# Optimization experiments

Hardware: AMD Instinct MI355X
Metric: run time of the kernel (lower is better)

Reference implementation:

```python
import jax, jax.numpy as jnp
import numpy as np

MASK_VALUE = -1000000.0  # matches torch source's value=-1000000.0


def setup_inputs() -> dict:
    key = jax.random.key(0)
    kq, kk, kv, kl = jax.random.split(key, 4)
    B, S, D = 64, 1024, 64
    q = jax.random.normal(kq, (B, S, D), dtype=jnp.float32)
    k = jax.random.normal(kk, (B, S, D), dtype=jnp.float32)
    v = jax.random.normal(kv, (B, S, D), dtype=jnp.float32)
    valid_lens = jax.random.randint(kl, (B,), 0, S, dtype=jnp.int32)
    return {"q": q, "k": k, "v": v, "valid_lens": valid_lens}


def reference(q, k, v, valid_lens):
    # scores: [B, Sq, Sk]
    d = q.shape[-1]
    scores = jnp.einsum("bqd,bkd->bqk", q, k) / jnp.sqrt(jnp.float32(d))
    # 1-D valid_lens broadcast over the query dim (torch repeat_interleave branch)
    Sk = k.shape[1]
    mask = jnp.arange(Sk, dtype=jnp.int32)[None, None, :] < valid_lens[:, None, None]
    scores = jnp.where(mask, scores, MASK_VALUE)
    attn = jax.nn.softmax(scores, axis=-1)
    # dropout p=0.0 -> identity (eval-mode reference)
    return jnp.einsum("bqk,bkd->bqd", attn, v)
```

## Files before the change

### kernel.cpp

```cpp
#include <hip/hip_runtime.h>
#include <math.h>


#define BATCH 64
#define SEQ   1024
#define DIM   64
#define BQ    128
#define BC    64
#define NKT   (SEQ / BC)
#define LSTR  72

#define MASK_VALUE -1000000.0f

typedef __attribute__((ext_vector_type(8))) short bf16x8;
typedef __attribute__((ext_vector_type(4))) float f32x4;

__device__ __forceinline__ ushort f2bf(float x) {
    union { float f; uint u; } v; v.f = x;
    uint u = v.u;
    return (ushort)((u + 0x7fffu + ((u >> 16) & 1u)) >> 16);
}

__global__ __launch_bounds__(256, 2) void attn_mfma_flash(
    const float* __restrict__ q, const float* __restrict__ k,
    const float* __restrict__ v, const int* __restrict__ valid_lens,
    float* __restrict__ out)
{
    __shared__ ushort Qs[BQ * LSTR];
    __shared__ ushort Ks[BC * LSTR];
    __shared__ ushort Vt[DIM * LSTR];
    __shared__ ushort Ps[BQ * LSTR];

    const int t    = threadIdx.x;
    const int wave = t >> 6;
    const int wl   = t & 63;
    const int QD   = wl >> 4;
    const int li   = wl & 15;
    const int b    = blockIdx.x >> 3;
    const int q0   = (blockIdx.x & 7) * BQ;
    const int vl   = valid_lens[b];
    const int qw   = wave * 32;

    const size_t boff = (size_t)b * SEQ * DIM;

    {
        const float4* qg = (const float4*)(q + boff + (size_t)q0 * DIM);
        #pragma unroll
        for (int i = 0; i < 8; i++) {
            int idx = t + 256 * i;
            int row = idx >> 4;
            int c4  = idx & 15;
            float4 val = qg[idx];
            ushort4 pk;
            pk.x = f2bf(val.x); pk.y = f2bf(val.y);
            pk.z = f2bf(val.z); pk.w = f2bf(val.w);
            *(ushort4*)&Qs[row * LSTR + c4 * 4] = pk;
        }
    }

    const int it_max = (vl == 0) ? NKT : ((vl + BC - 1) >> 6);

    float m_run[2] = {-INFINITY, -INFINITY};
    float l_run[2] = {0.f, 0.f};
    f32x4 acc_o[2][4];
    #pragma unroll
    for (int a = 0; a < 2; a++)
        #pragma unroll
        for (int d = 0; d < 4; d++)
            acc_o[a][d] = (f32x4){0.f, 0.f, 0.f, 0.f};

    for (int it = 0; it < it_max; it++) {
        __syncthreads();

        {
            const float4* kg = (const float4*)(k + boff + (size_t)it * BC * DIM);
            #pragma unroll
            for (int i = 0; i < 4; i++) {
                int idx = t + 256 * i;
                int row = idx >> 4;
                int c4  = idx & 15;
                float4 val = kg[idx];
                ushort4 pk;
                pk.x = f2bf(val.x); pk.y = f2bf(val.y);
                pk.z = f2bf(val.z); pk.w = f2bf(val.w);
                *(ushort4*)&Ks[row * LSTR + c4 * 4] = pk;
            }
            const float4* vg = (const float4*)(v + boff + (size_t)it * BC * DIM);
            #pragma unroll
            for (int i = 0; i < 2; i++) {
                int slot = t + 256 * i;
                int kp = slot >> 4;
                int c4 = slot & 15;
                float4 v0 = vg[(2 * kp) * 16 + c4];
                float4 v1 = vg[(2 * kp + 1) * 16 + c4];
                ushort2 w0 = {f2bf(v0.x), f2bf(v1.x)};
                ushort2 w1 = {f2bf(v0.y), f2bf(v1.y)};
                ushort2 w2 = {f2bf(v0.z), f2bf(v1.z)};
                ushort2 w3 = {f2bf(v0.w), f2bf(v1.w)};
                *(ushort2*)&Vt[(c4 * 4 + 0) * LSTR + 2 * kp] = w0;
                *(ushort2*)&Vt[(c4 * 4 + 1) * LSTR + 2 * kp] = w1;
                *(ushort2*)&Vt[(c4 * 4 + 2) * LSTR + 2 * kp] = w2;
                *(ushort2*)&Vt[(c4 * 4 + 3) * LSTR + 2 * kp] = w3;
            }
        }
        __syncthreads();

        f32x4 sc[4][2];
        {
            bf16x8 qb[2][2], ka[4][2];
            #pragma unroll
            for (int nt = 0; nt < 2; nt++)
                #pragma unroll
                for (int kc = 0; kc < 2; kc++)
                    qb[nt][kc] = *(const bf16x8*)&Qs[(qw + nt * 16 + li) * LSTR + kc * 32 + QD * 8];
            #pragma unroll
            for (int kt = 0; kt < 4; kt++)
                #pragma unroll
                for (int kc = 0; kc < 2; kc++)
                    ka[kt][kc] = *(const bf16x8*)&Ks[(kt * 16 + li) * LSTR + kc * 32 + QD * 8];
            #pragma unroll
            for (int kt = 0; kt < 4; kt++)
                #pragma unroll
                for (int nt = 0; nt < 2; nt++) {
                    f32x4 c = (f32x4){0.f, 0.f, 0.f, 0.f};
                    c = __builtin_amdgcn_mfma_f32_16x16x32_bf16(ka[kt][0], qb[nt][0], c, 0, 0, 0);
                    c = __builtin_amdgcn_mfma_f32_16x16x32_bf16(ka[kt][1], qb[nt][1], c, 0, 0, 0);
                    sc[kt][nt] = c;
                }
        }

        const int kbase = it * BC;
        float mt_[2] = {-INFINITY, -INFINITY};
        #pragma unroll
        for (int kt = 0; kt < 4; kt++)
            #pragma unroll
            for (int nt = 0; nt < 2; nt++)
                #pragma unroll
                for (int r = 0; r < 4; r++) {
                    int key = kbase + kt * 16 + QD * 4 + r;
                    float x = (key < vl) ? sc[kt][nt][r] * 0.125f : MASK_VALUE;
                    sc[kt][nt][r] = x;
                    mt_[nt] = fmaxf(mt_[nt], x);
                }
        #pragma unroll
        for (int nt = 0; nt < 2; nt++) {
            mt_[nt] = fmaxf(mt_[nt], __shfl_xor(mt_[nt], 16, 64));
            mt_[nt] = fmaxf(mt_[nt], __shfl_xor(mt_[nt], 32, 64));
        }

        float alpha[2], ls[2];
        #pragma unroll
        for (int nt = 0; nt < 2; nt++) {
            float mn = fmaxf(m_run[nt], mt_[nt]);
            alpha[nt] = __expf(m_run[nt] - mn);
            m_run[nt] = mn;
            ls[nt] = 0.f;
        }

        #pragma unroll
        for (int kt = 0; kt < 4; kt++)
            #pragma unroll
            for (int nt = 0; nt < 2; nt++) {
                float p0 = __expf(sc[kt][nt][0] - m_run[nt]);
                float p1 = __expf(sc[kt][nt][1] - m_run[nt]);
                float p2 = __expf(sc[kt][nt][2] - m_run[nt]);
                float p3 = __expf(sc[kt][nt][3] - m_run[nt]);
                ls[nt] += (p0 + p1) + (p2 + p3);
                ushort4 pk = {f2bf(p0), f2bf(p1), f2bf(p2), f2bf(p3)};
                *(ushort4*)&Ps[(qw + nt * 16 + li) * LSTR + kt * 16 + QD * 4] = pk;
            }

        #pragma unroll
        for (int nt = 0; nt < 2; nt++) {
            ls[nt] += __shfl_xor(ls[nt], 16, 64);
            ls[nt] += __shfl_xor(ls[nt], 32, 64);
            l_run[nt] = l_run[nt] * alpha[nt] + ls[nt];
        }

        #pragma unroll
        for (int qt = 0; qt < 2; qt++) {
            float a0 = __shfl(alpha[qt], QD * 4 + 0, 64);
            float a1 = __shfl(alpha[qt], QD * 4 + 1, 64);
            float a2 = __shfl(alpha[qt], QD * 4 + 2, 64);
            float a3 = __shfl(alpha[qt], QD * 4 + 3, 64);
            #pragma unroll
            for (int dt = 0; dt < 4; dt++) {
                acc_o[qt][dt][0] *= a0;
                acc_o[qt][dt][1] *= a1;
                acc_o[qt][dt][2] *= a2;
                acc_o[qt][dt][3] *= a3;
            }
        }

        {
            bf16x8 pa[2][2], vb[4][2];
            #pragma unroll
            for (int qt = 0; qt < 2; qt++)
                #pragma unroll
                for (int kc = 0; kc < 2; kc++)
                    pa[qt][kc] = *(const bf16x8*)&Ps[(qw + qt * 16 + li) * LSTR + kc * 32 + QD * 8];
            #pragma unroll
            for (int dt = 0; dt < 4; dt++)
                #pragma unroll
                for (int kc = 0; kc < 2; kc++)
                    vb[dt][kc] = *(const bf16x8*)&Vt[(dt * 16 + li) * LSTR + kc * 32 + QD * 8];
            #pragma unroll
            for (int qt = 0; qt < 2; qt++)
                #pragma unroll
                for (int dt = 0; dt < 4; dt++) {
                    acc_o[qt][dt] = __builtin_amdgcn_mfma_f32_16x16x32_bf16(pa[qt][0], vb[dt][0], acc_o[qt][dt], 0, 0, 0);
                    acc_o[qt][dt] = __builtin_amdgcn_mfma_f32_16x16x32_bf16(pa[qt][1], vb[dt][1], acc_o[qt][dt], 0, 0, 0);
                }
        }
    }

    float invl[2];
    #pragma unroll
    for (int qt = 0; qt < 2; qt++) invl[qt] = 1.0f / l_run[qt];

    float* ob = out + boff + (size_t)q0 * DIM;
    #pragma unroll
    for (int qt = 0; qt < 2; qt++) {
        float i0 = __shfl(invl[qt], QD * 4 + 0, 64);
        float i1 = __shfl(invl[qt], QD * 4 + 1, 64);
        float i2 = __shfl(invl[qt], QD * 4 + 2, 64);
        float i3 = __shfl(invl[qt], QD * 4 + 3, 64);
        #pragma unroll
        for (int dt = 0; dt < 4; dt++) {
            int col = dt * 16 + li;
            ob[(size_t)(qw + qt * 16 + QD * 4 + 0) * DIM + col] = acc_o[qt][dt][0] * i0;
            ob[(size_t)(qw + qt * 16 + QD * 4 + 1) * DIM + col] = acc_o[qt][dt][1] * i1;
            ob[(size_t)(qw + qt * 16 + QD * 4 + 2) * DIM + col] = acc_o[qt][dt][2] * i2;
            ob[(size_t)(qw + qt * 16 + QD * 4 + 3) * DIM + col] = acc_o[qt][dt][3] * i3;
        }
    }
}

extern "C" void kernel_launch(void* const* d_in, const int* in_sizes, int n_in,
                              void* d_out, int out_size, void* d_ws, size_t ws_size,
                              hipStream_t stream) {
    const float* q = (const float*)d_in[0];
    const float* k = (const float*)d_in[1];
    const float* v = (const float*)d_in[2];
    const int* valid_lens = (const int*)d_in[3];
    float* out = (float*)d_out;

    dim3 grid(BATCH * (SEQ / BQ));
    dim3 block(256);
    attn_mfma_flash<<<grid, block, 0, stream>>>(q, k, v, valid_lens, out);
}
```

Before: 137.2 us.

## Rewrite flash attention with register-prefetched K/V tiles, smaller Q block, exp2 softmax

```diff
diff --git a/kernel.cpp b/kernel.cpp
--- a/kernel.cpp
+++ b/kernel.cpp
@@ -5,28 +5,29 @@
 #define BATCH 64
 #define SEQ   1024
 #define DIM   64
-#define BQ    128
+#define BQ    64
 #define BC    64
 #define NKT   (SEQ / BC)
 #define LSTR  72
-
-#define MASK_VALUE -1000000.0f
+#define QSCALE 0.18033688011112442f
+#define MASKED -1.0e6f
 
 typedef __attribute__((ext_vector_type(8))) short bf16x8;
 typedef __attribute__((ext_vector_type(4))) float f32x4;
 
-__device__ __forceinline__ ushort f2bf(float x) {
-    union { float f; uint u; } v; v.f = x;
-    uint u = v.u;
+__device__ __forceinline__ uint pack2_trunc(float lo, float hi) {
+    return __builtin_amdgcn_perm(__float_as_uint(hi), __float_as_uint(lo), 0x07060302);
+}
+__device__ __forceinline__ ushort f2bf_rne(float x) {
+    uint u = __float_as_uint(x);
     return (ushort)((u + 0x7fffu + ((u >> 16) & 1u)) >> 16);
 }
 
-__global__ __launch_bounds__(256, 2) void attn_mfma_flash(
+__global__ __launch_bounds__(256, 4) void attn_mfma_flash2(
     const float* __restrict__ q, const float* __restrict__ k,
     const float* __restrict__ v, const int* __restrict__ valid_lens,
     float* __restrict__ out)
 {
-    __shared__ ushort Qs[BQ * LSTR];
     __shared__ ushort Ks[BC * LSTR];
     __shared__ ushort Vt[DIM * LSTR];
     __shared__ ushort Ps[BQ * LSTR];
@@ -36,203 +37,173 @@
     const int wl   = t & 63;
     const int QD   = wl >> 4;
     const int li   = wl & 15;
-    const int b    = blockIdx.x >> 3;
-    const int q0   = (blockIdx.x & 7) * BQ;
+    const int b    = blockIdx.x & 63;
+    const int q0   = (blockIdx.x >> 6) * BQ;
     const int vl   = valid_lens[b];
-    const int qw   = wave * 32;
 
     const size_t boff = (size_t)b * SEQ * DIM;
 
+    bf16x8 qb[2];
     {
-        const float4* qg = (const float4*)(q + boff + (size_t)q0 * DIM);
-        #pragma unroll
-        for (int i = 0; i < 8; i++) {
+        const float* qrow = q + boff + (size_t)(q0 + wave * 16 + li) * DIM + QD * 8;
+        #pragma unroll
+        for (int kc = 0; kc < 2; kc++) {
+            float4 a = *(const float4*)(qrow + kc * 32);
+            float4 c = *(const float4*)(qrow + kc * 32 + 4);
+            union { bf16x8 v; ushort u[8]; } tmp;
+            tmp.u[0] = f2bf_rne(a.x * QSCALE);
+            tmp.u[1] = f2bf_rne(a.y * QSCALE);
+            tmp.u[2] = f2bf_rne(a.z * QSCALE);
+            tmp.u[3] = f2bf_rne(a.w * QSCALE);
+            tmp.u[4] = f2bf_rne(c.x * QSCALE);
+            tmp.u[5] = f2bf_rne(c.y * QSCALE);
+            tmp.u[6] = f2bf_rne(c.z * QSCALE);
+            tmp.u[7] = f2bf_rne(c.w * QSCALE);
+            qb[kc] = tmp.v;
+        }
+    }
+
+    const int it_max = (vl == 0) ? NKT : ((vl + BC - 1) >> 6);
+
+    float4 kf[4];
+    float  vf[2][8];
+
+    auto load_tile = [&](int it) {
+        const float4* kg = (const float4*)(k + boff + (size_t)it * BC * DIM);
+        #pragma unroll
+        for (int i = 0; i < 4; i++) kf[i] = kg[t + 256 * i];
+        const float* vgf = v + boff + (size_t)it * BC * DIM;
+        #pragma unroll
+        for (int i = 0; i < 2; i++) {
+            int slot = t + 256 * i;
+            int d = slot & 63, ko = slot >> 6;
+            #pragma unroll
+            for (int j = 0; j < 8; j++)
+                vf[i][j] = vgf[(size_t)(ko * 8 + j) * DIM + d];
+        }
+    };
+
+    auto stage = [&]() {
+        #pragma unroll
+        for (int i = 0; i < 4; i++) {
             int idx = t + 256 * i;
-            int row = idx >> 4;
-            int c4  = idx & 15;
-            float4 val = qg[idx];
-            ushort4 pk;
-            pk.x = f2bf(val.x); pk.y = f2bf(val.y);
-            pk.z = f2bf(val.z); pk.w = f2bf(val.w);
-            *(ushort4*)&Qs[row * LSTR + c4 * 4] = pk;
-        }
-    }
-
-    const int it_max = (vl == 0) ? NKT : ((vl + BC - 1) >> 6);
-
-    float m_run[2] = {-INFINITY, -INFINITY};
-    float l_run[2] = {0.f, 0.f};
-    f32x4 acc_o[2][4];
+            int row = idx >> 4, c4 = idx & 15;
+            uint2 w;
+            w.x = pack2_trunc(kf[i].x, kf[i].y);
+            w.y = pack2_trunc(kf[i].z, kf[i].w);
+            *(uint2*)&Ks[row * LSTR + c4 * 4] = w;
+        }
+        #pragma unroll
+        for (int i = 0; i < 2; i++) {
+            int slot = t + 256 * i;
+            int d = slot & 63, ko = slot >> 6;
+            uint4 w;
+            w.x = pack2_trunc(vf[i][0], vf[i][1]);
+            w.y = pack2_trunc(vf[i][2], vf[i][3]);
+            w.z = pack2_trunc(vf[i][4], vf[i][5]);
+            w.w = pack2_trunc(vf[i][6], vf[i][7]);
+            *(uint4*)&Vt[d * LSTR + ko * 8] = w;
+        }
+    };
+
+    float m_run = -INFINITY, l_run = 0.f;
+    f32x4 acc[4];
     #pragma unroll
-    for (int a = 0; a < 2; a++)
-        #pragma unroll
-        for (int d = 0; d < 4; d++)
-            acc_o[a][d] = (f32x4){0.f, 0.f, 0.f, 0.f};
+    for (int dt = 0; dt < 4; dt++) acc[dt] = (f32x4){0.f, 0.f, 0.f, 0.f};
+
+    load_tile(0);
 
     for (int it = 0; it < it_max; it++) {
         __syncthreads();
-
-        {
-            const float4* kg = (const float4*)(k + boff + (size_t)it * BC * DIM);
-            #pragma unroll
-            for (int i = 0; i < 4; i++) {
-                int idx = t + 256 * i;
-                int row = idx >> 4;
-                int c4  = idx & 15;
-                float4 val = kg[idx];
-                ushort4 pk;
-                pk.x = f2bf(val.x); pk.y = f2bf(val.y);
-                pk.z = f2bf(val.z); pk.w = f2bf(val.w);
-                *(ushort4*)&Ks[row * LSTR + c4 * 4] = pk;
-            }
-            const float4* vg = (const float4*)(v + boff + (size_t)it * BC * DIM);
-            #pragma unroll
-            for (int i = 0; i < 2; i++) {
-                int slot = t + 256 * i;
-                int kp = slot >> 4;
-                int c4 = slot & 15;
-                float4 v0 = vg[(2 * kp) * 16 + c4];
-                float4 v1 = vg[(2 * kp + 1) * 16 + c4];
-                ushort2 w0 = {f2bf(v0.x), f2bf(v1.x)};
-                ushort2 w1 = {f2bf(v0.y), f2bf(v1.y)};
-                ushort2 w2 = {f2bf(v0.z), f2bf(v1.z)};
-                ushort2 w3 = {f2bf(v0.w), f2bf(v1.w)};
-                *(ushort2*)&Vt[(c4 * 4 + 0) * LSTR + 2 * kp] = w0;
-                *(ushort2*)&Vt[(c4 * 4 + 1) * LSTR + 2 * kp] = w1;
-                *(ushort2*)&Vt[(c4 * 4 + 2) * LSTR + 2 * kp] = w2;
-                *(ushort2*)&Vt[(c4 * 4 + 3) * LSTR + 2 * kp] = w3;
-            }
-        }
+        stage();
+        if (it + 1 < it_max) load_tile(it + 1);
         __syncthreads();
 
-        f32x4 sc[4][2];
-        {
-            bf16x8 qb[2][2], ka[4][2];
-            #pragma unroll
-            for (int nt = 0; nt < 2; nt++)
-                #pragma unroll
-                for (int kc = 0; kc < 2; kc++)
-                    qb[nt][kc] = *(const bf16x8*)&Qs[(qw + nt * 16 + li) * LSTR + kc * 32 + QD * 8];
+        f32x4 sc[4];
+        #pragma unroll
+        for (int kt = 0; kt < 4; kt++) {
+            bf16x8 ka0 = *(const bf16x8*)&Ks[(kt * 16 + li) * LSTR + QD * 8];
+            bf16x8 ka1 = *(const bf16x8*)&Ks[(kt * 16 + li) * LSTR + 32 + QD * 8];
+            f32x4 c = (f32x4){0.f, 0.f, 0.f, 0.f};
+            c = __builtin_amdgcn_mfma_f32_16x16x32_bf16(ka0, qb[0], c, 0, 0, 0);
+            c = __builtin_amdgcn_mfma_f32_16x16x32_bf16(ka1, qb[1], c, 0, 0, 0);
+            sc[kt] = c;
+        }
+
+        const int kbase = it * BC;
+        if (kbase + BC > vl) {
             #pragma unroll
             for (int kt = 0; kt < 4; kt++)
                 #pragma unroll
-                for (int kc = 0; kc < 2; kc++)
-                    ka[kt][kc] = *(const bf16x8*)&Ks[(kt * 16 + li) * LSTR + kc * 32 + QD * 8];
-            #pragma unroll
-            for (int kt = 0; kt < 4; kt++)
-                #pragma unroll
-                for (int nt = 0; nt < 2; nt++) {
-                    f32x4 c = (f32x4){0.f, 0.f, 0.f, 0.f};
-                    c = __builtin_amdgcn_mfma_f32_16x16x32_bf16(ka[kt][0], qb[nt][0], c, 0, 0, 0);
-                    c = __builtin_amdgcn_mfma_f32_16x16x32_bf16(ka[kt][1], qb[nt][1], c, 0, 0, 0);
-                    sc[kt][nt] = c;
+                for (int r = 0; r < 4; r++) {
+                    int key = kbase + kt * 16 + QD * 4 + r;
+                    if (key >= vl) sc[kt][r] = MASKED;
                 }
         }
 
-        const int kbase = it * BC;
-        float mt_[2] = {-INFINITY, -INFINITY};
+        float mt = -INFINITY;
         #pragma unroll
         for (int kt = 0; kt < 4; kt++)
             #pragma unroll
-            for (int nt = 0; nt < 2; nt++)
-                #pragma unroll
-                for (int r = 0; r < 4; r++) {
-                    int key = kbase + kt * 16 + QD * 4 + r;
-                    float x = (key < vl) ? sc[kt][nt][r] * 0.125f : MASK_VALUE;
-                    sc[kt][nt][r] = x;
-                    mt_[nt] = fmaxf(mt_[nt], x);
-                }
-        #pragma unroll
-        for (int nt = 0; nt < 2; nt++) {
-            mt_[nt] = fmaxf(mt_[nt], __shfl_xor(mt_[nt], 16, 64));
-            mt_[nt] = fmaxf(mt_[nt], __shfl_xor(mt_[nt], 32, 64));
-        }
-
-        float alpha[2], ls[2];
-        #pragma unroll
-        for (int nt = 0; nt < 2; nt++) {
-            float mn = fmaxf(m_run[nt], mt_[nt]);
-            alpha[nt] = __expf(m_run[nt] - mn);
-            m_run[nt] = mn;
-            ls[nt] = 0.f;
-        }
-
-        #pragma unroll
-        for (int kt = 0; kt < 4; kt++)
-            #pragma unroll
-            for (int nt = 0; nt < 2; nt++) {
-                float p0 = __expf(sc[kt][nt][0] - m_run[nt]);
-                float p1 = __expf(sc[kt][nt][1] - m_run[nt]);
-                float p2 = __expf(sc[kt][nt][2] - m_run[nt]);
-                float p3 = __expf(sc[kt][nt][3] - m_run[nt]);
-                ls[nt] += (p0 + p1) + (p2 + p3);
-                ushort4 pk = {f2bf(p0), f2bf(p1), f2bf(p2), f2bf(p3)};
-                *(ushort4*)&Ps[(qw + nt * 16 + li) * LSTR + kt * 16 + QD * 4] = pk;
-            }
-
-        #pragma unroll
-        for (int nt = 0; nt < 2; nt++) {
-            ls[nt] += __shfl_xor(ls[nt], 16, 64);
-            ls[nt] += __shfl_xor(ls[nt], 32, 64);
-            l_run[nt] = l_run[nt] * alpha[nt] + ls[nt];
-        }
-
-        #pragma unroll
-        for (int qt = 0; qt < 2; qt++) {
-            float a0 = __shfl(alpha[qt], QD * 4 + 0, 64);
-            float a1 = __shfl(alpha[qt], QD * 4 + 1, 64);
-            float a2 = __shfl(alpha[qt], QD * 4 + 2, 64);
-            float a3 = __shfl(alpha[qt], QD * 4 + 3, 64);
-            #pragma unroll
-            for (int dt = 0; dt < 4; dt++) {
-                acc_o[qt][dt][0] *= a0;
-                acc_o[qt][dt][1] *= a1;
-                acc_o[qt][dt][2] *= a2;
-                acc_o[qt][dt][3] *= a3;
-            }
-        }
-
-        {
-            bf16x8 pa[2][2], vb[4][2];
-            #pragma unroll
-            for (int qt = 0; qt < 2; qt++)
-                #pragma unroll
-                for (int kc = 0; kc < 2; kc++)
-                    pa[qt][kc] = *(const bf16x8*)&Ps[(qw + qt * 16 + li) * LSTR + kc * 32 + QD * 8];
-            #pragma unroll
-            for (int dt = 0; dt < 4; dt++)
-                #pragma unroll
-                for (int kc = 0; kc < 2; kc++)
-                    vb[dt][kc] = *(const bf16x8*)&Vt[(dt * 16 + li) * LSTR + kc * 32 + QD * 8];
-            #pragma unroll
-            for (int qt = 0; qt < 2; qt++)
-                #pragma unroll
-                for (int dt = 0; dt < 4; dt++) {
-                    acc_o[qt][dt] = __builtin_amdgcn_mfma_f32_16x16x32_bf16(pa[qt][0], vb[dt][0], acc_o[qt][dt], 0, 0, 0);
-                    acc_o[qt][dt] = __builtin_amdgcn_mfma_f32_16x16x32_bf16(pa[qt][1], vb[dt][1], acc_o[qt][dt], 0, 0, 0);
-                }
+            for (int r = 0; r < 4; r++) mt = fmaxf(mt, sc[kt][r]);
+        mt = fmaxf(mt, __shfl_xor(mt, 16, 64));
+        mt = fmaxf(mt, __shfl_xor(mt, 32, 64));
+        float mn = fmaxf(m_run, mt);
+        float alpha = exp2f(m_run - mn);
+        m_run = mn;
+
+        float ls = 0.f;
+        #pragma unroll
+        for (int kt = 0; kt < 4; kt++) {
+            float p0 = exp2f(sc[kt][0] - mn);
+            float p1 = exp2f(sc[kt][1] - mn);
+            float p2 = exp2f(sc[kt][2] - mn);
+            float p3 = exp2f(sc[kt][3] - mn);
+            ls += (p0 + p1) + (p2 + p3);
+            uint2 w;
+            w.x = pack2_trunc(p0, p1);
+            w.y = pack2_trunc(p2, p3);
+            *(uint2*)&Ps[(wave * 16 + li) * LSTR + kt * 16 + QD * 4] = w;
+        }
+        ls += __shfl_xor(ls, 16, 64);
+        ls += __shfl_xor(ls, 32, 64);
+        l_run = l_run * alpha + ls;
+
+        float a0 = __shfl(alpha, QD * 4 + 0, 64);
+        float a1 = __shfl(alpha, QD * 4 + 1, 64);
+        float a2 = __shfl(alpha, QD * 4 + 2, 64);
+        float a3 = __shfl(alpha, QD * 4 + 3, 64);
+        #pragma unroll
+        for (int dt = 0; dt < 4; dt++) {
+            acc[dt][0] *= a0; acc[dt][1] *= a1;
+            acc[dt][2] *= a2; acc[dt][3] *= a3;
+        }
+
+        bf16x8 pa0 = *(const bf16x8*)&Ps[(wave * 16 + li) * LSTR + QD * 8];
+        bf16x8 pa1 = *(const bf16x8*)&Ps[(wave * 16 + li) * LSTR + 32 + QD * 8];
+        #pragma unroll
+        for (int dt = 0; dt < 4; dt++) {
+            bf16x8 vb0 = *(const bf16x8*)&Vt[(dt * 16 + li) * LSTR + QD * 8];
+            bf16x8 vb1 = *(const bf16x8*)&Vt[(dt * 16 + li) * LSTR + 32 + QD * 8];
+            acc[dt] = __builtin_amdgcn_mfma_f32_16x16x32_bf16(pa0, vb0, acc[dt], 0, 0, 0);
+            acc[dt] = __builtin_amdgcn_mfma_f32_16x16x32_bf16(pa1, vb1, acc[dt], 0, 0, 0);
         }
     }
 
-    float invl[2];
+    float invl = 1.0f / l_run;
+    float i0 = __shfl(invl, QD * 4 + 0, 64);
+    float i1 = __shfl(invl, QD * 4 + 1, 64);
+    float i2 = __shfl(invl, QD * 4 + 2, 64);
+    float i3 = __shfl(invl, QD * 4 + 3, 64);
+    float* ob = out + boff + (size_t)q0 * DIM;
+    const int rbase = wave * 16 + QD * 4;
     #pragma unroll
-    for (int qt = 0; qt < 2; qt++) invl[qt] = 1.0f / l_run[qt];
-
-    float* ob = out + boff + (size_t)q0 * DIM;
-    #pragma unroll
-    for (int qt = 0; qt < 2; qt++) {
-        float i0 = __shfl(invl[qt], QD * 4 + 0, 64);
-        float i1 = __shfl(invl[qt], QD * 4 + 1, 64);
-        float i2 = __shfl(invl[qt], QD * 4 + 2, 64);
-        float i3 = __shfl(invl[qt], QD * 4 + 3, 64);
-        #pragma unroll
-        for (int dt = 0; dt < 4; dt++) {
-            int col = dt * 16 + li;
-            ob[(size_t)(qw + qt * 16 + QD * 4 + 0) * DIM + col] = acc_o[qt][dt][0] * i0;
-            ob[(size_t)(qw + qt * 16 + QD * 4 + 1) * DIM + col] = acc_o[qt][dt][1] * i1;
-            ob[(size_t)(qw + qt * 16 + QD * 4 + 2) * DIM + col] = acc_o[qt][dt][2] * i2;
-            ob[(size_t)(qw + qt * 16 + QD * 4 + 3) * DIM + col] = acc_o[qt][dt][3] * i3;
-        }
+    for (int dt = 0; dt < 4; dt++) {
+        int col = dt * 16 + li;
+        ob[(size_t)(rbase + 0) * DIM + col] = acc[dt][0] * i0;
+        ob[(size_t)(rbase + 1) * DIM + col] = acc[dt][1] * i1;
+        ob[(size_t)(rbase + 2) * DIM + col] = acc[dt][2] * i2;
+        ob[(size_t)(rbase + 3) * DIM + col] = acc[dt][3] * i3;
     }
 }
 
@@ -247,5 +218,5 @@
 
     dim3 grid(BATCH * (SEQ / BQ));
     dim3 block(256);
-    attn_mfma_flash<<<grid, block, 0, stream>>>(q, k, v, valid_lens, out);
-}
+    attn_mfma_flash2<<<grid, block, 0, stream>>>(q, k, v, valid_lens, out);
+}
```

Result: faster. 127.5 us (-7.0%).
